# Optimization experiments

Hardware: AMD Instinct MI355X
Metric: run time of the kernel (lower is better)

Reference implementation:

```python
import jax, jax.numpy as jnp
from jax import lax
import numpy as np

B, T, C, W = 128, 64, 64, 27
H, K = 128, 3
EPS = 1e-5


def _conv1d(x, w, b):
    # x: (N, Cin, W), w: (Cout, Cin, K) -> (N, Cout, W), 'same' padding
    y = lax.conv_general_dilated(x, w, (1,), 'SAME', dimension_numbers=('NCH', 'OIH', 'NCH'))
    return y + b[None, :, None]


def _mish(x):
    return x * jnp.tanh(jax.nn.softplus(x))


def _gru_layer(x_seq, act_seq, gw, gb, cw, cb, aw, ab, bn_g, bn_b):
    # x_seq: (T, B, Cin, W); act_seq: (T, B, 8, W)
    Hd = bn_g.shape[0]

    def step(h, xa):
        x, a = xa
        gates = _conv1d(jnp.concatenate([x, h], axis=1), gw, gb)  # (B, 2H, W)
        reset = jax.nn.sigmoid(gates[:, :Hd])
        update = jax.nn.sigmoid(gates[:, Hd:])
        cnm = _conv1d(jnp.concatenate([x, reset * h], axis=1), cw, cb) + _conv1d(a, aw, ab)
        pre = _mish((1.0 - update) * h + update * cnm)
        # BatchNorm1d (training mode): per-channel stats over (batch, width)
        mean = pre.mean(axis=(0, 2), keepdims=True)
        var = pre.var(axis=(0, 2), keepdims=True)
        h_next = bn_g[None, :, None] * (pre - mean) * lax.rsqrt(var + EPS) + bn_b[None, :, None]
        return h_next, h_next

    h0 = jnp.zeros((x_seq.shape[1], Hd, x_seq.shape[3]), dtype=x_seq.dtype)
    _, ys = lax.scan(step, h0, (x_seq, act_seq))
    return ys  # (T, B, H, W)


def setup_inputs():
    key = jax.random.key(0)
    ks = jax.random.split(key, 16)
    s = 0.05
    d = {}
    d['input_tensor'] = jax.random.normal(ks[0], (B, T, C, W), dtype=jnp.float32)
    # layer 0 (cur_input_dim = C)
    d['gates_w0'] = jax.random.normal(ks[1], (2 * H, C + H, K)) * s
    d['gates_b0'] = jnp.zeros((2 * H,))
    d['can_w0'] = jax.random.normal(ks[2], (H, C + H, K)) * s
    d['can_b0'] = jnp.zeros((H,))
    d['cond_w0'] = jax.random.normal(ks[3], (H, 8, K)) * s
    d['cond_b0'] = jnp.zeros((H,))
    d['bn_g0'] = jnp.ones((H,))
    d['bn_b0'] = jnp.zeros((H,))
    # layer 1 (cur_input_dim = H)
    d['gates_w1'] = jax.random.normal(ks[4], (2 * H, H + H, K)) * s
    d['gates_b1'] = jnp.zeros((2 * H,))
    d['can_w1'] = jax.random.normal(ks[5], (H, H + H, K)) * s
    d['can_b1'] = jnp.zeros((H,))
    d['cond_w1'] = jax.random.normal(ks[6], (H, 8, K)) * s
    d['cond_b1'] = jnp.zeros((H,))
    d['bn_g1'] = jnp.ones((H,))
    d['bn_b1'] = jnp.zeros((H,))
    # concentrate linear: (27*H) -> 1
    d['conc_w'] = jax.random.normal(ks[7], (1, W * H)) * s
    d['conc_b'] = jnp.zeros((1,))
    return d


def reference(input_tensor, gates_w0, gates_b0, can_w0, can_b0, cond_w0, cond_b0, bn_g0, bn_b0,
              gates_w1, gates_b1, can_w1, can_b1, cond_w1, cond_b1, bn_g1, bn_b1, conc_w, conc_b):
    x_t = jnp.transpose(input_tensor, (1, 0, 2, 3))  # (T, B, C, W)
    act_t = x_t[:, :, -8:, :]                        # (T, B, 8, W)
    h1 = _gru_layer(x_t, act_t, gates_w0, gates_b0, can_w0, can_b0, cond_w0, cond_b0, bn_g0, bn_b0)
    h2 = _gru_layer(h1, act_t, gates_w1, gates_b1, can_w1, can_b1, cond_w1, cond_b1, bn_g1, bn_b1)
    # (T, B, H, W) -> (B, T, H*W)
    out = jnp.transpose(h2, (1, 0, 2, 3)).reshape(input_tensor.shape[0], input_tensor.shape[1], -1)
    reward = out @ conc_w.T[:, 0] + conc_b[0]        # (B, T)
    return 0.99 * (reward[:, -1] - reward[:, -2])
```

## Files before the change

kernel.cpp:

```cpp
#include <hip/hip_runtime.h>
#include <math.h>

#define Bn 128
#define Tn 64
#define Cn 64
#define Wn 27
#define Hn 128
#define EPSf 1e-5f
#define NBWf 3456.0f

struct Params {
  const float* in;
  const float4* wt_g0; const float* gb0;
  const float4* wt_c0; const float* cb0;
  const float4* wt_a0; const float* ab0;
  const float* bg0; const float* bb0;
  const float4* wt_g1; const float* gb1;
  const float4* wt_c1; const float* cb1;
  const float4* wt_a1; const float* ab1;
  const float* bg1; const float* bb1;
  const float* concw;
  float* pre1a; float* pre1b; float* pre2a; float* pre2b;
  float* sums;
  unsigned* cnt;
  float* out;
};

__device__ __forceinline__ void bn_coef(const float* __restrict__ sums,
                                        const float* __restrict__ g,
                                        const float* __restrict__ b,
                                        int c, float& sc, float& sh) {
  float s1 = sums[2 * c], s2 = sums[2 * c + 1];
  float mean = s1 * (1.0f / NBWf);
  float var = s2 * (1.0f / NBWf) - mean * mean;
  sc = g[c] * rsqrtf(var + EPSf);
  sh = b[c] - mean * sc;
}

__device__ __forceinline__ float sigm(float x) {
  return 1.0f / (1.0f + __expf(-x));
}

__device__ __forceinline__ int swz(int row, int c) {
  return row * 32 + ((((c >> 2) ^ (row & 7)) & 7) << 2) + (c & 3);
}

__device__ __forceinline__ void conv_row(const float* __restrict__ rowbase,
                                         int sw, float w0, float w1, float w2,
                                         float* __restrict__ acc) {
  const float4* rp = (const float4*)rowbase;
  float xa[16];
  {
    float4 v0 = rp[0 ^ sw];
    float4 v1 = rp[1 ^ sw];
    float4 v2 = rp[2 ^ sw];
    float4 v3 = rp[3 ^ sw];
    xa[0] = v0.x; xa[1] = v0.y; xa[2] = v0.z; xa[3] = v0.w;
    xa[4] = v1.x; xa[5] = v1.y; xa[6] = v1.z; xa[7] = v1.w;
    xa[8] = v2.x; xa[9] = v2.y; xa[10] = v2.z; xa[11] = v2.w;
    xa[12] = v3.x; xa[13] = v3.y; xa[14] = v3.z; xa[15] = v3.w;
  }
#pragma unroll
  for (int c = 1; c <= 14; ++c)
    acc[c - 1] = fmaf(w2, xa[c + 1], fmaf(w1, xa[c], fmaf(w0, xa[c - 1], acc[c - 1])));
  float xc[15];
  xc[0] = xa[14]; xc[1] = xa[15];
  {
    float4 v4 = rp[4 ^ sw];
    float4 v5 = rp[5 ^ sw];
    float4 v6 = rp[6 ^ sw];
    float4 v7 = rp[7 ^ sw];
    xc[2] = v4.x; xc[3] = v4.y; xc[4] = v4.z; xc[5] = v4.w;
    xc[6] = v5.x; xc[7] = v5.y; xc[8] = v5.z; xc[9] = v5.w;
    xc[10] = v6.x; xc[11] = v6.y; xc[12] = v6.z; xc[13] = v6.w;
    xc[14] = v7.x;
  }
#pragma unroll
  for (int k = 0; k < 13; ++k)
    acc[14 + k] = fmaf(w2, xc[k + 2], fmaf(w1, xc[k + 1], fmaf(w0, xc[k], acc[14 + k])));
}

template <int IC, bool XN>
__device__ void step_body(const Params& p, int b, int t, bool hv,
    const float* __restrict__ xpre, const float* __restrict__ xs,
    const float* __restrict__ xg, const float* __restrict__ xb,
    const float* __restrict__ hpre, const float* __restrict__ hs,
    const float* __restrict__ hg, const float* __restrict__ hb,
    const float4* __restrict__ wtg, const float* __restrict__ gbias,
    const float4* __restrict__ wtc, const float* __restrict__ cbias,
    const float4* __restrict__ wta, const float* __restrict__ abias,
    float* __restrict__ pre_out, float* __restrict__ sums_out,
    float* lx, float* lrh, float* lu) {
  const int tid = threadIdx.x;
  constexpr int ROWS = IC + 136;
  {
    const int q = tid & 3;
    const int w0c = q * 7;
    const int wcnt = (q == 3) ? 6 : 7;
    for (int r = tid >> 2; r < ROWS; r += 256) {
      float sc = 1.f, sh = 0.f;
      const float* src = nullptr;
      if (r < IC) {
        if (XN) {
          bn_coef(xs, xg, xb, r, sc, sh);
          src = xpre + ((size_t)b * Hn + r) * Wn;
        } else {
          src = p.in + (((size_t)b * Tn + t) * Cn + r) * Wn;
        }
      } else if (r < IC + 128) {
        if (hv) {
          bn_coef(hs, hg, hb, r - IC, sc, sh);
          src = hpre + ((size_t)b * Hn + (r - IC)) * Wn;
        }
      } else {
        src = p.in + (((size_t)b * Tn + t) * Cn + 56 + (r - IC - 128)) * Wn;
      }
      if (q == 0) lx[swz(r, 0)] = 0.f;
      if (q == 3) {
        lx[swz(r, 28)] = 0.f; lx[swz(r, 29)] = 0.f;
        lx[swz(r, 30)] = 0.f; lx[swz(r, 31)] = 0.f;
      }
      if (src) {
        for (int j = 0; j < wcnt; ++j)
          lx[swz(r, 1 + w0c + j)] = src[w0c + j] * sc + sh;
      } else {
        for (int j = 0; j < wcnt; ++j) lx[swz(r, 1 + w0c + j)] = 0.f;
      }
    }
  }
  __syncthreads();
  {
    const int rc = tid & 3;
    const int och = tid >> 2;
    float acc[27];
#pragma unroll
    for (int j = 0; j < 27; ++j) acc[j] = 0.f;
    const int rows = hv ? IC + 128 : IC;
    for (int i = rc; i < rows; i += 4) {
      float4 w = wtg[i * 256 + och];
      conv_row(lx + i * 32, i & 7, w.x, w.y, w.z, acc);
    }
#pragma unroll
    for (int j = 0; j < 27; ++j) {
      acc[j] += __shfl_xor(acc[j], 1);
      acc[j] += __shfl_xor(acc[j], 2);
    }
    const float bias = gbias[och];
    if (och < 128) {
      if (rc == 0) {
        lrh[swz(och, 0)] = 0.f;
        lrh[swz(och, 28)] = 0.f; lrh[swz(och, 29)] = 0.f;
        lrh[swz(och, 30)] = 0.f; lrh[swz(och, 31)] = 0.f;
      }
#pragma unroll
      for (int j = rc; j < 27; j += 4) {
        float gv = sigm(acc[j] + bias);
        lrh[swz(och, j + 1)] = gv * lx[swz(IC + och, j + 1)];
      }
    } else {
      const int ch = och - 128;
#pragma unroll
      for (int j = rc; j < 27; j += 4)
        lu[ch * 27 + j] = sigm(acc[j] + bias);
    }
  }
  __syncthreads();
  {
    const int rc8 = tid & 7;
    const int ch = tid >> 3;
    float acc[27];
#pragma unroll
    for (int j = 0; j < 27; ++j) acc[j] = 0.f;
    for (int i = rc8; i < IC; i += 8) {
      float4 w = wtc[i * 128 + ch];
      conv_row(lx + i * 32, i & 7, w.x, w.y, w.z, acc);
    }
    if (hv) {
      for (int i = rc8; i < 128; i += 8) {
        float4 w = wtc[(IC + i) * 128 + ch];
        conv_row(lrh + i * 32, i & 7, w.x, w.y, w.z, acc);
      }
    }
    {
      const int i = rc8;
      float4 w = wta[i * 128 + ch];
      const int r = IC + 128 + i;
      conv_row(lx + r * 32, r & 7, w.x, w.y, w.z, acc);
    }
#pragma unroll
    for (int j = 0; j < 27; ++j) {
      acc[j] += __shfl_xor(acc[j], 1);
      acc[j] += __shfl_xor(acc[j], 2);
      acc[j] += __shfl_xor(acc[j], 4);
    }
    const float cb = cbias[ch] + abias[ch];
    float s1 = 0.f, s2 = 0.f;
#pragma unroll
    for (int j = rc8; j < 27; j += 8) {
      float u = lu[ch * 27 + j];
      float hn = lx[swz(IC + ch, j + 1)];
      float z = (1.f - u) * hn + u * (acc[j] + cb);
      float pv;
      if (z > 20.f) {
        pv = z;
      } else {
        float q = 1.f + __expf(z);
        float q2 = q * q;
        pv = z * (q2 - 1.f) / (q2 + 1.f);
      }
      pre_out[((size_t)b * Hn + ch) * Wn + j] = pv;
      s1 += pv;
      s2 += pv * pv;
    }
    s1 += __shfl_xor(s1, 1); s2 += __shfl_xor(s2, 1);
    s1 += __shfl_xor(s1, 2); s2 += __shfl_xor(s2, 2);
    s1 += __shfl_xor(s1, 4); s2 += __shfl_xor(s2, 4);
    if (rc8 == 0) {
      atomicAdd(&sums_out[2 * ch], s1);
      atomicAdd(&sums_out[2 * ch + 1], s2);
    }
  }
}

__device__ __forceinline__ void gbar(unsigned* cnt, unsigned target) {
  __syncthreads();
  if (threadIdx.x == 0) {
    __threadfence();
    atomicAdd(cnt, 1u);
    while (__hip_atomic_load(cnt, __ATOMIC_RELAXED, __HIP_MEMORY_SCOPE_AGENT) < target) {
      __builtin_amdgcn_s_sleep(8);
    }
    __threadfence();
  }
  __syncthreads();
}

__global__ __launch_bounds__(1024, 1) void k_all(Params p) {
  __shared__ __align__(16) float lx[264 * 32];
  __shared__ __align__(16) float lrh[128 * 32];
  __shared__ float lu[128 * 27];
  const int bid = blockIdx.x;
  const bool L1b = (bid & 7) >= 4;
  const int b = (bid >> 3) * 4 + (bid & 3);
  float* pre1[2] = {p.pre1a, p.pre1b};
  float* pre2[2] = {p.pre2a, p.pre2b};
  for (int ph = 0; ph < 65; ++ph) {
    if (!L1b) {
      if (ph < 64) {
        const int t = ph;
        const bool hv = t > 0;
        step_body<Cn, false>(p, b, t, hv,
            nullptr, nullptr, nullptr, nullptr,
            hv ? pre1[(t - 1) & 1] : nullptr,
            hv ? p.sums + (size_t)(t - 1) * 256 : nullptr, p.bg0, p.bb0,
            p.wt_g0, p.gb0, p.wt_c0, p.cb0, p.wt_a0, p.ab0,
            pre1[t & 1], p.sums + (size_t)t * 256, lx, lrh, lu);
      }
    } else {
      if (ph >= 1) {
        const int t = ph - 1;
        const bool hv = t > 0;
        step_body<Hn, true>(p, b, t, hv,
            pre1[t & 1], p.sums + (size_t)t * 256, p.bg0, p.bb0,
            hv ? pre2[(t - 1) & 1] : nullptr,
            hv ? p.sums + (size_t)(64 + t - 1) * 256 : nullptr, p.bg1, p.bb1,
            p.wt_g1, p.gb1, p.wt_c1, p.cb1, p.wt_a1, p.ab1,
            pre2[t & 1], p.sums + (size_t)(64 + t) * 256, lx, lrh, lu);
      }
    }
    gbar(p.cnt, (unsigned)(ph + 1) * 256u);
  }
  if (!L1b) {
    const float* p63 = pre2[1];
    const float* p62 = pre2[0];
    const float* s63 = p.sums + (size_t)(64 + 63) * 256;
    const float* s62 = p.sums + (size_t)(64 + 62) * 256;
    const int tid = threadIdx.x;
    float acc = 0.f;
    for (int idx = tid; idx < Hn * Wn; idx += 1024) {
      int o = idx / Wn;
      float sc3, sh3, sc2, sh2;
      bn_coef(s63, p.bg1, p.bb1, o, sc3, sh3);
      bn_coef(s62, p.bg1, p.bb1, o, sc2, sh2);
      float v3 = p63[(size_t)b * Hn * Wn + idx] * sc3 + sh3;
      float v2 = p62[(size_t)b * Hn * Wn + idx] * sc2 + sh2;
      acc += (v3 - v2) * p.concw[idx];
    }
    lx[tid] = acc;
    __syncthreads();
    for (int s = 512; s > 0; s >>= 1) {
      if (tid < s) lx[tid] += lx[tid + s];
      __syncthreads();
    }
    if (tid == 0) p.out[b] = 0.99f * lx[0];
  }
}

__global__ void k_twt4(const float* __restrict__ src, float4* __restrict__ dst,
                       int M, int IC) {
  int idx = blockIdx.x * 256 + threadIdx.x;
  int total = M * IC;
  if (idx >= total) return;
  int i = idx / M;
  int o = idx - i * M;
  const float* s = src + ((size_t)o * IC + i) * 3;
  dst[idx] = make_float4(s[0], s[1], s[2], 0.f);
}

extern "C" void kernel_launch(void* const* d_in, const int* in_sizes, int n_in,
                              void* d_out, int out_size, void* d_ws,
                              size_t ws_size, hipStream_t stream) {
  const float* in = (const float*)d_in[0];
  const float* gw0 = (const float*)d_in[1];
  const float* gb0 = (const float*)d_in[2];
  const float* cw0 = (const float*)d_in[3];
  const float* cb0 = (const float*)d_in[4];
  const float* aw0 = (const float*)d_in[5];
  const float* ab0 = (const float*)d_in[6];
  const float* bg0 = (const float*)d_in[7];
  const float* bb0 = (const float*)d_in[8];
  const float* gw1 = (const float*)d_in[9];
  const float* gb1 = (const float*)d_in[10];
  const float* cw1 = (const float*)d_in[11];
  const float* cb1 = (const float*)d_in[12];
  const float* aw1 = (const float*)d_in[13];
  const float* ab1 = (const float*)d_in[14];
  const float* bg1 = (const float*)d_in[15];
  const float* bb1 = (const float*)d_in[16];
  const float* concw = (const float*)d_in[17];
  float* out = (float*)d_out;

  float* ws = (float*)d_ws;
  size_t off = 0;
  float4* wt_g0 = (float4*)(ws + off); off += 4 * 192 * 256;
  float4* wt_c0 = (float4*)(ws + off); off += 4 * 192 * 128;
  float4* wt_a0 = (float4*)(ws + off); off += 4 * 8 * 128;
  float4* wt_g1 = (float4*)(ws + off); off += 4 * 256 * 256;
  float4* wt_c1 = (float4*)(ws + off); off += 4 * 256 * 128;
  float4* wt_a1 = (float4*)(ws + off); off += 4 * 8 * 128;
  const size_t PRE = (size_t)Bn * Hn * Wn;
  float* pre1a = ws + off; off += PRE;
  float* pre1b = ws + off; off += PRE;
  float* pre2a = ws + off; off += PRE;
  float* pre2b = ws + off; off += PRE;
  float* sums = ws + off; off += 2 * 64 * 256;
  unsigned* cnt = (unsigned*)(ws + off); off += 16;
  if (ws_size < off * sizeof(float)) return;

  hipMemsetAsync(sums, 0, (2 * 64 * 256 + 16) * sizeof(float), stream);

  auto tw = [&](const float* s, float4* d, int M, int IC) {
    int tot = M * IC;
    k_twt4<<<(tot + 255) / 256, 256, 0, stream>>>(s, d, M, IC);
  };
  tw(gw0, wt_g0, 256, 192);
  tw(cw0, wt_c0, 128, 192);
  tw(aw0, wt_a0, 128, 8);
  tw(gw1, wt_g1, 256, 256);
  tw(cw1, wt_c1, 128, 256);
  tw(aw1, wt_a1, 128, 8);

  Params prm;
  prm.in = in;
  prm.wt_g0 = wt_g0; prm.gb0 = gb0;
  prm.wt_c0 = wt_c0; prm.cb0 = cb0;
  prm.wt_a0 = wt_a0; prm.ab0 = ab0;
  prm.bg0 = bg0; prm.bb0 = bb0;
  prm.wt_g1 = wt_g1; prm.gb1 = gb1;
  prm.wt_c1 = wt_c1; prm.cb1 = cb1;
  prm.wt_a1 = wt_a1; prm.ab1 = ab1;
  prm.bg1 = bg1; prm.bb1 = bb1;
  prm.concw = concw;
  prm.pre1a = pre1a; prm.pre1b = pre1b;
  prm.pre2a = pre2a; prm.pre2b = pre2b;
  prm.sums = sums; prm.cnt = cnt; prm.out = out;

  k_all<<<256, 1024, 0, stream>>>(prm);
}
```

Before: 7.194 ms.

## Register-block two output channels per thread and fold cond conv into candidate weights

Each thread now accumulates two output channels per input row in both the gate and the candidate convolutions. Every LDS row read is therefore reused for twice the FMAs, and the row-split reduction widens to 8 and 16 lanes. The cond (action) conv weights are packed as extra rows of the candidate weight matrix, so a single loop covers x, reset*h and action rows. The cost is higher register pressure from two 27-wide accumulators, and at t=0 the gate loop now also processes the zero h rows unconditionally.

```diff
diff --git a/kernel.cpp b/kernel.cpp
--- a/kernel.cpp
+++ b/kernel.cpp
@@ -12,12 +12,10 @@
 struct Params {
   const float* in;
   const float4* wt_g0; const float* gb0;
-  const float4* wt_c0; const float* cb0;
-  const float4* wt_a0; const float* ab0;
+  const float4* wt_c0; const float* cb0; const float* ab0;
   const float* bg0; const float* bb0;
   const float4* wt_g1; const float* gb1;
-  const float4* wt_c1; const float* cb1;
-  const float4* wt_a1; const float* ab1;
+  const float4* wt_c1; const float* cb1; const float* ab1;
   const float* bg1; const float* bb1;
   const float* concw;
   float* pre1a; float* pre1b; float* pre2a; float* pre2b;
@@ -45,9 +43,9 @@
   return row * 32 + ((((c >> 2) ^ (row & 7)) & 7) << 2) + (c & 3);
 }
 
-__device__ __forceinline__ void conv_row(const float* __restrict__ rowbase,
-                                         int sw, float w0, float w1, float w2,
-                                         float* __restrict__ acc) {
+__device__ __forceinline__ void conv_row2(const float* __restrict__ rowbase,
+                                          int sw, float4 wA, float4 wB,
+                                          float (*__restrict__ acc)[27]) {
   const float4* rp = (const float4*)rowbase;
   float xa[16];
   {
@@ -61,8 +59,10 @@
     xa[12] = v3.x; xa[13] = v3.y; xa[14] = v3.z; xa[15] = v3.w;
   }
 #pragma unroll
-  for (int c = 1; c <= 14; ++c)
-    acc[c - 1] = fmaf(w2, xa[c + 1], fmaf(w1, xa[c], fmaf(w0, xa[c - 1], acc[c - 1])));
+  for (int c = 1; c <= 14; ++c) {
+    acc[0][c - 1] = fmaf(wA.z, xa[c + 1], fmaf(wA.y, xa[c], fmaf(wA.x, xa[c - 1], acc[0][c - 1])));
+    acc[1][c - 1] = fmaf(wB.z, xa[c + 1], fmaf(wB.y, xa[c], fmaf(wB.x, xa[c - 1], acc[1][c - 1])));
+  }
   float xc[15];
   xc[0] = xa[14]; xc[1] = xa[15];
   {
@@ -76,8 +76,10 @@
     xc[14] = v7.x;
   }
 #pragma unroll
-  for (int k = 0; k < 13; ++k)
-    acc[14 + k] = fmaf(w2, xc[k + 2], fmaf(w1, xc[k + 1], fmaf(w0, xc[k], acc[14 + k])));
+  for (int k = 0; k < 13; ++k) {
+    acc[0][14 + k] = fmaf(wA.z, xc[k + 2], fmaf(wA.y, xc[k + 1], fmaf(wA.x, xc[k], acc[0][14 + k])));
+    acc[1][14 + k] = fmaf(wB.z, xc[k + 2], fmaf(wB.y, xc[k + 1], fmaf(wB.x, xc[k], acc[1][14 + k])));
+  }
 }
 
 template <int IC, bool XN>
@@ -88,7 +90,7 @@
     const float* __restrict__ hg, const float* __restrict__ hb,
     const float4* __restrict__ wtg, const float* __restrict__ gbias,
     const float4* __restrict__ wtc, const float* __restrict__ cbias,
-    const float4* __restrict__ wta, const float* __restrict__ abias,
+    const float* __restrict__ abias,
     float* __restrict__ pre_out, float* __restrict__ sums_out,
     float* lx, float* lrh, float* lu) {
   const int tid = threadIdx.x;
@@ -130,94 +132,114 @@
   }
   __syncthreads();
   {
-    const int rc = tid & 3;
-    const int och = tid >> 2;
-    float acc[27];
-#pragma unroll
-    for (int j = 0; j < 27; ++j) acc[j] = 0.f;
-    const int rows = hv ? IC + 128 : IC;
-    for (int i = rc; i < rows; i += 4) {
-      float4 w = wtg[i * 256 + och];
-      conv_row(lx + i * 32, i & 7, w.x, w.y, w.z, acc);
-    }
-#pragma unroll
-    for (int j = 0; j < 27; ++j) {
-      acc[j] += __shfl_xor(acc[j], 1);
-      acc[j] += __shfl_xor(acc[j], 2);
-    }
-    const float bias = gbias[och];
-    if (och < 128) {
+    const int g = tid >> 3;
+    const int rc = tid & 7;
+    float acc[2][27];
+#pragma unroll
+    for (int o = 0; o < 2; ++o)
+#pragma unroll
+      for (int j = 0; j < 27; ++j) acc[o][j] = 0.f;
+    constexpr int GR = IC + 128;
+    for (int i = rc; i < GR; i += 8) {
+      const float4* wp = wtg + i * 256 + 2 * g;
+      conv_row2(lx + i * 32, i & 7, wp[0], wp[1], acc);
+    }
+#pragma unroll
+    for (int o = 0; o < 2; ++o)
+#pragma unroll
+      for (int j = 0; j < 27; ++j) {
+        float v = acc[o][j];
+        v += __shfl_xor(v, 1);
+        v += __shfl_xor(v, 2);
+        v += __shfl_xor(v, 4);
+        acc[o][j] = v;
+      }
+    const float b0 = gbias[2 * g], b1 = gbias[2 * g + 1];
+    if (g < 64) {
+      const int r0 = 2 * g, r1 = 2 * g + 1;
       if (rc == 0) {
-        lrh[swz(och, 0)] = 0.f;
-        lrh[swz(och, 28)] = 0.f; lrh[swz(och, 29)] = 0.f;
-        lrh[swz(och, 30)] = 0.f; lrh[swz(och, 31)] = 0.f;
-      }
-#pragma unroll
-      for (int j = rc; j < 27; j += 4) {
-        float gv = sigm(acc[j] + bias);
-        lrh[swz(och, j + 1)] = gv * lx[swz(IC + och, j + 1)];
+        lrh[swz(r0, 0)] = 0.f;
+        lrh[swz(r0, 28)] = 0.f; lrh[swz(r0, 29)] = 0.f;
+        lrh[swz(r0, 30)] = 0.f; lrh[swz(r0, 31)] = 0.f;
+        lrh[swz(r1, 0)] = 0.f;
+        lrh[swz(r1, 28)] = 0.f; lrh[swz(r1, 29)] = 0.f;
+        lrh[swz(r1, 30)] = 0.f; lrh[swz(r1, 31)] = 0.f;
+      }
+#pragma unroll
+      for (int j = rc; j < 27; j += 8) {
+        float gv0 = sigm(acc[0][j] + b0);
+        float gv1 = sigm(acc[1][j] + b1);
+        lrh[swz(r0, j + 1)] = gv0 * lx[swz(IC + r0, j + 1)];
+        lrh[swz(r1, j + 1)] = gv1 * lx[swz(IC + r1, j + 1)];
       }
     } else {
-      const int ch = och - 128;
-#pragma unroll
-      for (int j = rc; j < 27; j += 4)
-        lu[ch * 27 + j] = sigm(acc[j] + bias);
+      const int ch = 2 * (g - 64);
+#pragma unroll
+      for (int j = rc; j < 27; j += 8) {
+        lu[ch * 27 + j] = sigm(acc[0][j] + b0);
+        lu[(ch + 1) * 27 + j] = sigm(acc[1][j] + b1);
+      }
     }
   }
   __syncthreads();
   {
-    const int rc8 = tid & 7;
-    const int ch = tid >> 3;
-    float acc[27];
-#pragma unroll
-    for (int j = 0; j < 27; ++j) acc[j] = 0.f;
-    for (int i = rc8; i < IC; i += 8) {
-      float4 w = wtc[i * 128 + ch];
-      conv_row(lx + i * 32, i & 7, w.x, w.y, w.z, acc);
-    }
-    if (hv) {
-      for (int i = rc8; i < 128; i += 8) {
-        float4 w = wtc[(IC + i) * 128 + ch];
-        conv_row(lrh + i * 32, i & 7, w.x, w.y, w.z, acc);
-      }
-    }
-    {
-      const int i = rc8;
-      float4 w = wta[i * 128 + ch];
-      const int r = IC + 128 + i;
-      conv_row(lx + r * 32, r & 7, w.x, w.y, w.z, acc);
-    }
-#pragma unroll
-    for (int j = 0; j < 27; ++j) {
-      acc[j] += __shfl_xor(acc[j], 1);
-      acc[j] += __shfl_xor(acc[j], 2);
-      acc[j] += __shfl_xor(acc[j], 4);
-    }
-    const float cb = cbias[ch] + abias[ch];
-    float s1 = 0.f, s2 = 0.f;
-#pragma unroll
-    for (int j = rc8; j < 27; j += 8) {
-      float u = lu[ch * 27 + j];
-      float hn = lx[swz(IC + ch, j + 1)];
-      float z = (1.f - u) * hn + u * (acc[j] + cb);
-      float pv;
-      if (z > 20.f) {
-        pv = z;
-      } else {
-        float q = 1.f + __expf(z);
-        float q2 = q * q;
-        pv = z * (q2 - 1.f) / (q2 + 1.f);
-      }
-      pre_out[((size_t)b * Hn + ch) * Wn + j] = pv;
-      s1 += pv;
-      s2 += pv * pv;
-    }
-    s1 += __shfl_xor(s1, 1); s2 += __shfl_xor(s2, 1);
-    s1 += __shfl_xor(s1, 2); s2 += __shfl_xor(s2, 2);
-    s1 += __shfl_xor(s1, 4); s2 += __shfl_xor(s2, 4);
-    if (rc8 == 0) {
-      atomicAdd(&sums_out[2 * ch], s1);
-      atomicAdd(&sums_out[2 * ch + 1], s2);
+    const int g2 = tid >> 4;
+    const int rc = tid & 15;
+    float acc[2][27];
+#pragma unroll
+    for (int o = 0; o < 2; ++o)
+#pragma unroll
+      for (int j = 0; j < 27; ++j) acc[o][j] = 0.f;
+    constexpr int NR = IC + 136;
+    for (int i = rc; i < NR; i += 16) {
+      const float* rb = (i >= IC && i < IC + 128) ? (lrh + (i - IC) * 32)
+                                                  : (lx + i * 32);
+      const float4* wp = wtc + i * 128 + 2 * g2;
+      conv_row2(rb, i & 7, wp[0], wp[1], acc);
+    }
+#pragma unroll
+    for (int o = 0; o < 2; ++o)
+#pragma unroll
+      for (int j = 0; j < 27; ++j) {
+        float v = acc[o][j];
+        v += __shfl_xor(v, 1);
+        v += __shfl_xor(v, 2);
+        v += __shfl_xor(v, 4);
+        v += __shfl_xor(v, 8);
+        acc[o][j] = v;
+      }
+    const int ch0 = 2 * g2, ch1 = 2 * g2 + 1;
+    const float cb0 = cbias[ch0] + abias[ch0];
+    const float cb1 = cbias[ch1] + abias[ch1];
+    float s10 = 0.f, s20 = 0.f, s11 = 0.f, s21 = 0.f;
+#pragma unroll
+    for (int j = rc; j < 27; j += 16) {
+      float u0 = lu[ch0 * 27 + j];
+      float u1 = lu[ch1 * 27 + j];
+      float hn0 = lx[swz(IC + ch0, j + 1)];
+      float hn1 = lx[swz(IC + ch1, j + 1)];
+      float z0 = (1.f - u0) * hn0 + u0 * (acc[0][j] + cb0);
+      float z1 = (1.f - u1) * hn1 + u1 * (acc[1][j] + cb1);
+      float pv0, pv1;
+      if (z0 > 20.f) pv0 = z0;
+      else { float q = 1.f + __expf(z0); float q2 = q * q; pv0 = z0 * (q2 - 1.f) / (q2 + 1.f); }
+      if (z1 > 20.f) pv1 = z1;
+      else { float q = 1.f + __expf(z1); float q2 = q * q; pv1 = z1 * (q2 - 1.f) / (q2 + 1.f); }
+      pre_out[((size_t)b * Hn + ch0) * Wn + j] = pv0;
+      pre_out[((size_t)b * Hn + ch1) * Wn + j] = pv1;
+      s10 += pv0; s20 += pv0 * pv0;
+      s11 += pv1; s21 += pv1 * pv1;
+    }
+#pragma unroll
+    for (int d = 1; d < 16; d <<= 1) {
+      s10 += __shfl_xor(s10, d); s20 += __shfl_xor(s20, d);
+      s11 += __shfl_xor(s11, d); s21 += __shfl_xor(s21, d);
+    }
+    if (rc == 0) {
+      atomicAdd(&sums_out[2 * ch0], s10);
+      atomicAdd(&sums_out[2 * ch0 + 1], s20);
+      atomicAdd(&sums_out[2 * ch1], s11);
+      atomicAdd(&sums_out[2 * ch1 + 1], s21);
     }
   }
 }
@@ -253,7 +275,7 @@
             nullptr, nullptr, nullptr, nullptr,
             hv ? pre1[(t - 1) & 1] : nullptr,
             hv ? p.sums + (size_t)(t - 1) * 256 : nullptr, p.bg0, p.bb0,
-            p.wt_g0, p.gb0, p.wt_c0, p.cb0, p.wt_a0, p.ab0,
+            p.wt_g0, p.gb0, p.wt_c0, p.cb0, p.ab0,
             pre1[t & 1], p.sums + (size_t)t * 256, lx, lrh, lu);
       }
     } else {
@@ -264,7 +286,7 @@
             pre1[t & 1], p.sums + (size_t)t * 256, p.bg0, p.bb0,
             hv ? pre2[(t - 1) & 1] : nullptr,
             hv ? p.sums + (size_t)(64 + t - 1) * 256 : nullptr, p.bg1, p.bb1,
-            p.wt_g1, p.gb1, p.wt_c1, p.cb1, p.wt_a1, p.ab1,
+            p.wt_g1, p.gb1, p.wt_c1, p.cb1, p.ab1,
             pre2[t & 1], p.sums + (size_t)(64 + t) * 256, lx, lrh, lu);
       }
     }
@@ -296,14 +318,16 @@
   }
 }
 
-__global__ void k_twt4(const float* __restrict__ src, float4* __restrict__ dst,
-                       int M, int IC) {
+__global__ void k_twt4(const float* __restrict__ src,
+                       const float* __restrict__ srcb,
+                       float4* __restrict__ dst, int M, int Rmain, int Rtot) {
   int idx = blockIdx.x * 256 + threadIdx.x;
-  int total = M * IC;
+  int total = M * Rtot;
   if (idx >= total) return;
   int i = idx / M;
   int o = idx - i * M;
-  const float* s = src + ((size_t)o * IC + i) * 3;
+  const float* s = (i < Rmain) ? src + ((size_t)o * Rmain + i) * 3
+                               : srcb + ((size_t)o * 8 + (i - Rmain)) * 3;
   dst[idx] = make_float4(s[0], s[1], s[2], 0.f);
 }
 
@@ -333,11 +357,9 @@
   float* ws = (float*)d_ws;
   size_t off = 0;
   float4* wt_g0 = (float4*)(ws + off); off += 4 * 192 * 256;
-  float4* wt_c0 = (float4*)(ws + off); off += 4 * 192 * 128;
-  float4* wt_a0 = (float4*)(ws + off); off += 4 * 8 * 128;
   float4* wt_g1 = (float4*)(ws + off); off += 4 * 256 * 256;
-  float4* wt_c1 = (float4*)(ws + off); off += 4 * 256 * 128;
-  float4* wt_a1 = (float4*)(ws + off); off += 4 * 8 * 128;
+  float4* wt_c0 = (float4*)(ws + off); off += 4 * 200 * 128;
+  float4* wt_c1 = (float4*)(ws + off); off += 4 * 264 * 128;
   const size_t PRE = (size_t)Bn * Hn * Wn;
   float* pre1a = ws + off; off += PRE;
   float* pre1b = ws + off; off += PRE;
@@ -349,26 +371,23 @@
 
   hipMemsetAsync(sums, 0, (2 * 64 * 256 + 16) * sizeof(float), stream);
 
-  auto tw = [&](const float* s, float4* d, int M, int IC) {
-    int tot = M * IC;
-    k_twt4<<<(tot + 255) / 256, 256, 0, stream>>>(s, d, M, IC);
+  auto tw = [&](const float* s, const float* sb, float4* d, int M, int Rm,
+                int Rt) {
+    int tot = M * Rt;
+    k_twt4<<<(tot + 255) / 256, 256, 0, stream>>>(s, sb, d, M, Rm, Rt);
   };
-  tw(gw0, wt_g0, 256, 192);
-  tw(cw0, wt_c0, 128, 192);
-  tw(aw0, wt_a0, 128, 8);
-  tw(gw1, wt_g1, 256, 256);
-  tw(cw1, wt_c1, 128, 256);
-  tw(aw1, wt_a1, 128, 8);
+  tw(gw0, nullptr, wt_g0, 256, 192, 192);
+  tw(gw1, nullptr, wt_g1, 256, 256, 256);
+  tw(cw0, aw0, wt_c0, 128, 192, 200);
+  tw(cw1, aw1, wt_c1, 128, 256, 264);
 
   Params prm;
   prm.in = in;
   prm.wt_g0 = wt_g0; prm.gb0 = gb0;
-  prm.wt_c0 = wt_c0; prm.cb0 = cb0;
-  prm.wt_a0 = wt_a0; prm.ab0 = ab0;
+  prm.wt_c0 = wt_c0; prm.cb0 = cb0; prm.ab0 = ab0;
   prm.bg0 = bg0; prm.bb0 = bb0;
   prm.wt_g1 = wt_g1; prm.gb1 = gb1;
-  prm.wt_c1 = wt_c1; prm.cb1 = cb1;
-  prm.wt_a1 = wt_a1; prm.ab1 = ab1;
+  prm.wt_c1 = wt_c1; prm.cb1 = cb1; prm.ab1 = ab1;
   prm.bg1 = bg1; prm.bb1 = bb1;
   prm.concw = concw;
   prm.pre1a = pre1a; prm.pre1b = pre1b;
```

New measurement: 8.919 ms. +24.0%, slower.
